# Performance work log

Hardware: AMD Instinct MI355X
Metric: run time of the kernel (lower is better)

## Reference

```python
import jax, jax.numpy as jnp
import numpy as np

N = 20000      # nodes
E = 320000     # edges (before self loops)
DIN = 64       # input feature dim
C = 256        # hidden_dim (per-head channels)
HEADS = 4
NEG_SLOPE_ATT = 0.2   # GATv2 leaky_relu slope
NEG_SLOPE = 0.01      # torch F.leaky_relu default


def setup_inputs() -> dict:
    key = jax.random.key(0)
    ks = jax.random.split(key, 32)
    def g(i, shape, fan_in):
        return jax.random.normal(ks[i], shape, jnp.float32) * (1.0 / np.sqrt(fan_in))
    inp = {}
    inp["x"] = jax.random.normal(ks[0], (N, DIN), jnp.float32)
    inp["src"] = jax.random.randint(ks[1], (E,), 0, N, jnp.int32)
    inp["dst"] = jax.random.randint(ks[2], (E,), 0, N, jnp.int32)
    # input layer
    inp["W_in"] = g(3, (DIN, C), DIN); inp["b_in"] = jnp.zeros((C,), jnp.float32)
    # conv1: in=256 -> heads=4, out=256, concat
    inp["Wl1"] = g(4, (C, HEADS * C), C); inp["bl1"] = jnp.zeros((HEADS * C,), jnp.float32)
    inp["Wr1"] = g(5, (C, HEADS * C), C); inp["br1"] = jnp.zeros((HEADS * C,), jnp.float32)
    inp["att1"] = g(6, (HEADS, C), C); inp["bias1"] = jnp.zeros((HEADS * C,), jnp.float32)
    # conv2: in=1024 -> heads=4, out=256, concat
    inp["Wl2"] = g(7, (HEADS * C, HEADS * C), HEADS * C); inp["bl2"] = jnp.zeros((HEADS * C,), jnp.float32)
    inp["Wr2"] = g(8, (HEADS * C, HEADS * C), HEADS * C); inp["br2"] = jnp.zeros((HEADS * C,), jnp.float32)
    inp["att2"] = g(9, (HEADS, C), C); inp["bias2"] = jnp.zeros((HEADS * C,), jnp.float32)
    # conv3: in=1024 -> heads=1, out=256, no concat
    inp["Wl3"] = g(10, (HEADS * C, C), HEADS * C); inp["bl3"] = jnp.zeros((C,), jnp.float32)
    inp["Wr3"] = g(11, (HEADS * C, C), HEADS * C); inp["br3"] = jnp.zeros((C,), jnp.float32)
    inp["att3"] = g(12, (1, C), C); inp["bias3"] = jnp.zeros((C,), jnp.float32)
    # output layer
    inp["W_out"] = g(13, (C, 1), C); inp["b_out"] = jnp.zeros((1,), jnp.float32)
    return inp


def _seg_softmax(scores, seg, n):
    # scores: [E, H] segment-wise softmax over dst node ids
    m = jax.ops.segment_max(scores, seg, num_segments=n)
    ex = jnp.exp(scores - m[seg])
    den = jax.ops.segment_sum(ex, seg, num_segments=n)
    return ex / den[seg]


def _gatv2(x, s, d, Wl, bl, Wr, br, att, bias, heads, concat):
    n = x.shape[0]
    c = att.shape[1]
    xl = (x @ Wl + bl).reshape(n, heads, c)  # messages (source side)
    xr = (x @ Wr + br).reshape(n, heads, c)  # target side
    e = jax.nn.leaky_relu(xl[s] + xr[d], NEG_SLOPE_ATT)          # [E, H, C]
    sc = jnp.einsum('ehc,hc->eh', e, att)                         # [E, H]
    alpha = _seg_softmax(sc, d, n)                                # [E, H]
    out = jax.ops.segment_sum(alpha[:, :, None] * xl[s], d, num_segments=n)  # [N, H, C]
    out = out.reshape(n, heads * c) if concat else out.mean(axis=1)
    return out + bias


def reference(x, src, dst, W_in, b_in, Wl1, bl1, Wr1, br1, att1, bias1,
              Wl2, bl2, Wr2, br2, att2, bias2, Wl3, bl3, Wr3, br3, att3, bias3,
              W_out, b_out):
    n = x.shape[0]
    loop = jnp.arange(n, dtype=src.dtype)
    s = jnp.concatenate([src, loop])  # add_self_loops=True (PyG default)
    d = jnp.concatenate([dst, loop])
    h = jax.nn.leaky_relu(x @ W_in + b_in, NEG_SLOPE)
    h1 = jax.nn.elu(_gatv2(h, s, d, Wl1, bl1, Wr1, br1, att1, bias1, HEADS, True))
    h2 = jax.nn.elu(_gatv2(h1, s, d, Wl2, bl2, Wr2, br2, att2, bias2, HEADS, True))
    h3 = _gatv2(h2, s, d, Wl3, bl3, Wr3, br3, att3, bias3, 1, False)
    out = jax.nn.leaky_relu(h3, NEG_SLOPE) + h
    logits = (out @ W_out + b_out).squeeze(-1)
    return logits
```

## Files before the change

kernel.cpp:

```cpp
#include <hip/hip_runtime.h>
#include <math.h>

#define NEG_ATT 0.2f
#define NEG 0.01f

typedef __attribute__((ext_vector_type(8))) short short8;
typedef __attribute__((ext_vector_type(4))) float f32x4;

static __device__ __forceinline__ float lrelu(float x, float s) { return x > 0.f ? x : s * x; }
static __device__ __forceinline__ unsigned short f2b(float f) {
  union { float f; unsigned int i; } v; v.f = f;
  unsigned int r = (v.i + 0x7fffu + ((v.i >> 16) & 1u)) >> 16;
  return (unsigned short)r;
}
static __device__ __forceinline__ void unpack8(uint4 r, float* x) {
  union { unsigned int u; float f; } t;
  t.u = r.x << 16;          x[0] = t.f;
  t.u = r.x & 0xffff0000u;  x[1] = t.f;
  t.u = r.y << 16;          x[2] = t.f;
  t.u = r.y & 0xffff0000u;  x[3] = t.f;
  t.u = r.z << 16;          x[4] = t.f;
  t.u = r.z & 0xffff0000u;  x[5] = t.f;
  t.u = r.w << 16;          x[6] = t.f;
  t.u = r.w & 0xffff0000u;  x[7] = t.f;
}
static __device__ __forceinline__ void async_copy16(const unsigned short* g, unsigned short* l) {
  __builtin_amdgcn_global_load_lds((const __attribute__((address_space(1))) unsigned int*)g,
                                   (__attribute__((address_space(3))) unsigned int*)l, 16, 0, 0);
}

__global__ void zero_int_kernel(int* __restrict__ p, int n) {
  int i = blockIdx.x * blockDim.x + threadIdx.x;
  if (i < n) p[i] = 0;
}

__global__ void hist_kernel(const int* __restrict__ dst, int* __restrict__ cnt, int E, int N) {
  int i = blockIdx.x * blockDim.x + threadIdx.x;
  int tot = E + N;
  if (i >= tot) return;
  int d = (i < E) ? dst[i] : (i - E);
  atomicAdd(&cnt[d], 1);
}

__global__ void scan_kernel(const int* __restrict__ cnt, int* __restrict__ rowptr,
                            int* __restrict__ cursor, int n) {
  __shared__ int wsum[16];
  __shared__ int carry_s;
  int t = threadIdx.x;
  int lane = t & 63, wv = t >> 6;
  if (t == 0) carry_s = 0;
  __syncthreads();
  for (int base = 0; base < n; base += 1024) {
    int i = base + t;
    int orig = (i < n) ? cnt[i] : 0;
    int v = orig;
    #pragma unroll
    for (int off = 1; off < 64; off <<= 1) {
      int u = __shfl_up(v, off);
      if (lane >= off) v += u;
    }
    if (lane == 63) wsum[wv] = v;
    __syncthreads();
    if (t < 16) {
      int s = wsum[t];
      #pragma unroll
      for (int off = 1; off < 16; off <<= 1) {
        int u = __shfl_up(s, off);
        if (t >= off) s += u;
      }
      wsum[t] = s;
    }
    __syncthreads();
    int waveoff = (wv > 0) ? wsum[wv - 1] : 0;
    int carry = carry_s;
    int excl = carry + waveoff + v - orig;
    if (i < n) { rowptr[i] = excl; cursor[i] = excl; }
    __syncthreads();
    if (t == 0) carry_s = carry + wsum[15];
    __syncthreads();
  }
  if (t == 0) rowptr[n] = carry_s;
}

__global__ void fill_kernel(const int* __restrict__ src, const int* __restrict__ dst,
                            int* __restrict__ cursor, int* __restrict__ colsrc, int E, int N) {
  int i = blockIdx.x * blockDim.x + threadIdx.x;
  int tot = E + N;
  if (i >= tot) return;
  int d, s;
  if (i < E) { d = dst[i]; s = src[i]; } else { d = i - E; s = i - E; }
  int pos = atomicAdd(&cursor[d], 1);
  colsrc[pos] = s;
}

__global__ __launch_bounds__(256) void transpose_w_bf16(
    const float* __restrict__ W, unsigned short* __restrict__ Wt, int K, int Ncol) {
  __shared__ float t[32][33];
  int n0 = blockIdx.x * 32, k0 = blockIdx.y * 32;
  int tx = threadIdx.x & 31, ty = threadIdx.x >> 5;
  #pragma unroll
  for (int i = 0; i < 4; ++i)
    t[ty + i * 8][tx] = W[(size_t)(k0 + ty + i * 8) * Ncol + n0 + tx];
  __syncthreads();
  #pragma unroll
  for (int i = 0; i < 4; ++i)
    Wt[(size_t)(n0 + ty + i * 8) * K + k0 + tx] = f2b(t[tx][ty + i * 8]);
}

__global__ void f2b_kernel(const float* __restrict__ in, unsigned short* __restrict__ out, int n) {
  int i = blockIdx.x * blockDim.x + threadIdx.x;
  if (i < n) out[i] = f2b(in[i]);
}

__global__ __launch_bounds__(256) void gemm_mfma(
    const unsigned short* __restrict__ A, const unsigned short* __restrict__ Bt,
    const float* __restrict__ bias, float* __restrict__ Cf, unsigned short* __restrict__ Cb,
    int M, int K, int ldcf, int ldcb, int act) {
  __shared__ __align__(16) unsigned short As[128][32];
  __shared__ __align__(16) unsigned short Bs[128][32];
  int tid = threadIdx.x;
  int wave = tid >> 6, lane = tid & 63;
  int wm = wave >> 1, wn = wave & 1;
  int quad = lane >> 4, l16 = lane & 15;
  int row0 = blockIdx.y * 128, col0 = blockIdx.x * 128;
  int lrow = lane >> 2, lseg = lane & 3;

  const unsigned short* gA = A + (size_t)(row0 + wave * 32 + lrow) * K + lseg * 8;
  const unsigned short* gB = Bt + (size_t)(col0 + wave * 32 + lrow) * K + lseg * 8;
  unsigned short* lA0 = &As[wave * 32][0];
  unsigned short* lA1 = &As[wave * 32 + 16][0];
  unsigned short* lB0 = &Bs[wave * 32][0];
  unsigned short* lB1 = &Bs[wave * 32 + 16][0];
  const size_t rstep = (size_t)16 * K;

  f32x4 acc[4][4];
  #pragma unroll
  for (int i = 0; i < 4; ++i)
    #pragma unroll
    for (int j = 0; j < 4; ++j)
      acc[i][j] = (f32x4){0.f, 0.f, 0.f, 0.f};

  for (int k0 = 0; k0 < K; k0 += 32) {
    async_copy16(gA + k0, lA0);
    async_copy16(gA + k0 + rstep, lA1);
    async_copy16(gB + k0, lB0);
    async_copy16(gB + k0 + rstep, lB1);
    __syncthreads();
    short8 afr[4], bfr[4];
    #pragma unroll
    for (int t = 0; t < 4; ++t) {
      afr[t] = *(const short8*)&As[wm * 64 + t * 16 + l16][quad * 8];
      bfr[t] = *(const short8*)&Bs[wn * 64 + t * 16 + l16][quad * 8];
    }
    #pragma unroll
    for (int mt = 0; mt < 4; ++mt)
      #pragma unroll
      for (int nt = 0; nt < 4; ++nt)
        acc[mt][nt] = __builtin_amdgcn_mfma_f32_16x16x32_bf16(afr[mt], bfr[nt], acc[mt][nt], 0, 0, 0);
    __syncthreads();
  }

  #pragma unroll
  for (int mt = 0; mt < 4; ++mt) {
    #pragma unroll
    for (int r = 0; r < 4; ++r) {
      int row = row0 + wm * 64 + mt * 16 + quad * 4 + r;
      if (row >= M) continue;
      #pragma unroll
      for (int nt = 0; nt < 4; ++nt) {
        int col = col0 + wn * 64 + nt * 16 + l16;
        float v = acc[mt][nt][r] + bias[col];
        if (act == 1) v = lrelu(v, NEG);
        if (Cf) Cf[(size_t)row * ldcf + col] = v;
        if (Cb) Cb[(size_t)row * ldcb + col] = f2b(v);
      }
    }
  }
}

__global__ __launch_bounds__(256) void gat_agg_h4(
    const unsigned short* __restrict__ xlr,
    const int* __restrict__ rowptr, const int* __restrict__ colsrc,
    const float* __restrict__ att, const float* __restrict__ bias,
    unsigned short* __restrict__ outb, int n) {
  const int S = 2048, XROFF = 1024;
  int d = blockIdx.x;
  if (d >= n) return;
  int hd = threadIdx.x >> 6, ln = threadIdx.x & 63;
  int half = ln >> 5, l32 = ln & 31;
  int c0 = l32 * 8;
  float a[8], a5[8], xr_[8];
  {
    float4 t0 = *(const float4*)(att + hd * 256 + c0);
    float4 t1 = *(const float4*)(att + hd * 256 + c0 + 4);
    a[0]=t0.x; a[1]=t0.y; a[2]=t0.z; a[3]=t0.w;
    a[4]=t1.x; a[5]=t1.y; a[6]=t1.z; a[7]=t1.w;
    #pragma unroll
    for (int c = 0; c < 8; ++c) a5[c] = NEG_ATT * a[c];
    uint4 r = *(const uint4*)(xlr + (size_t)d * S + XROFF + hd * 256 + c0);
    unpack8(r, xr_);
  }
  float m = -1e30f, l = 0.f, acc[8];
  #pragma unroll
  for (int c = 0; c < 8; ++c) acc[c] = 0.f;
  int beg = rowptr[d], end = rowptr[d + 1];
  for (int j = beg; j < end; j += 2) {
    int jj = j + half;
    bool valid = (jj < end);
    int s = colsrc[valid ? jj : j];
    uint4 raw = *(const uint4*)(xlr + (size_t)s * S + hd * 256 + c0);
    float x[8];
    unpack8(raw, x);
    float p = 0.f;
    #pragma unroll
    for (int c = 0; c < 8; ++c) {
      float u = x[c] + xr_[c];
      p = fmaf(u, (u > 0.f ? a[c] : a5[c]), p);
    }
    #pragma unroll
    for (int off = 16; off >= 1; off >>= 1) p += __shfl_xor(p, off);
    if (!valid) p = -1e30f;
    float nm = fmaxf(m, p);
    if (nm > m) {
      float scl = __expf(m - nm);
      l *= scl;
      #pragma unroll
      for (int c = 0; c < 8; ++c) acc[c] *= scl;
      m = nm;
    }
    float w = __expf(p - m);
    l += w;
    #pragma unroll
    for (int c = 0; c < 8; ++c) acc[c] = fmaf(w, x[c], acc[c]);
  }
  float mo = __shfl_xor(m, 32);
  float lo = __shfl_xor(l, 32);
  float M = fmaxf(m, mo);
  float sl = __expf(m - M);
  float so = __expf(mo - M);
  float L = fmaf(l, sl, lo * so);
  float inv = 1.f / L;
  float4 b0 = *(const float4*)(bias + hd * 256 + c0);
  float4 b1 = *(const float4*)(bias + hd * 256 + c0 + 4);
  float bb[8] = {b0.x, b0.y, b0.z, b0.w, b1.x, b1.y, b1.z, b1.w};
  unsigned int ou[4];
  #pragma unroll
  for (int c = 0; c < 8; ++c) {
    float po = __shfl_xor(acc[c], 32);
    float v = fmaf(acc[c], sl, po * so) * inv + bb[c];
    v = v > 0.f ? v : expm1f(v);
    unsigned int bv = (unsigned int)f2b(v);
    if (c & 1) ou[c >> 1] |= bv << 16; else ou[c >> 1] = bv;
  }
  if (half == 0) {
    uint4 o = make_uint4(ou[0], ou[1], ou[2], ou[3]);
    *(uint4*)(outb + (size_t)d * 1024 + hd * 256 + c0) = o;
  }
}

__global__ __launch_bounds__(256) void gat_agg_h1(
    const unsigned short* __restrict__ xlr,
    const int* __restrict__ rowptr, const int* __restrict__ colsrc,
    const float* __restrict__ att, const float* __restrict__ bias,
    float* __restrict__ out, int n) {
  const int S = 512, XROFF = 256;
  int wv = threadIdx.x >> 6, ln = threadIdx.x & 63;
  int d = blockIdx.x * 4 + wv;
  if (d >= n) return;
  int half = ln >> 5, l32 = ln & 31;
  int c0 = l32 * 8;
  float a[8], a5[8], xr_[8];
  {
    float4 t0 = *(const float4*)(att + c0);
    float4 t1 = *(const float4*)(att + c0 + 4);
    a[0]=t0.x; a[1]=t0.y; a[2]=t0.z; a[3]=t0.w;
    a[4]=t1.x; a[5]=t1.y; a[6]=t1.z; a[7]=t1.w;
    #pragma unroll
    for (int c = 0; c < 8; ++c) a5[c] = NEG_ATT * a[c];
    uint4 r = *(const uint4*)(xlr + (size_t)d * S + XROFF + c0);
    unpack8(r, xr_);
  }
  float m = -1e30f, l = 0.f, acc[8];
  #pragma unroll
  for (int c = 0; c < 8; ++c) acc[c] = 0.f;
  int beg = rowptr[d], end = rowptr[d + 1];
  for (int j = beg; j < end; j += 2) {
    int jj = j + half;
    bool valid = (jj < end);
    int s = colsrc[valid ? jj : j];
    uint4 raw = *(const uint4*)(xlr + (size_t)s * S + c0);
    float x[8];
    unpack8(raw, x);
    float p = 0.f;
    #pragma unroll
    for (int c = 0; c < 8; ++c) {
      float u = x[c] + xr_[c];
      p = fmaf(u, (u > 0.f ? a[c] : a5[c]), p);
    }
    #pragma unroll
    for (int off = 16; off >= 1; off >>= 1) p += __shfl_xor(p, off);
    if (!valid) p = -1e30f;
    float nm = fmaxf(m, p);
    if (nm > m) {
      float scl = __expf(m - nm);
      l *= scl;
      #pragma unroll
      for (int c = 0; c < 8; ++c) acc[c] *= scl;
      m = nm;
    }
    float w = __expf(p - m);
    l += w;
    #pragma unroll
    for (int c = 0; c < 8; ++c) acc[c] = fmaf(w, x[c], acc[c]);
  }
  float mo = __shfl_xor(m, 32);
  float lo = __shfl_xor(l, 32);
  float M = fmaxf(m, mo);
  float sl = __expf(m - M);
  float so = __expf(mo - M);
  float L = fmaf(l, sl, lo * so);
  float inv = 1.f / L;
  float4 b0 = *(const float4*)(bias + c0);
  float4 b1 = *(const float4*)(bias + c0 + 4);
  float bb[8] = {b0.x, b0.y, b0.z, b0.w, b1.x, b1.y, b1.z, b1.w};
  float ov[8];
  #pragma unroll
  for (int c = 0; c < 8; ++c) {
    float po = __shfl_xor(acc[c], 32);
    ov[c] = fmaf(acc[c], sl, po * so) * inv + bb[c];
  }
  if (half == 0) {
    float4 o0 = {ov[0], ov[1], ov[2], ov[3]};
    float4 o1 = {ov[4], ov[5], ov[6], ov[7]};
    *(float4*)(out + (size_t)d * 256 + c0) = o0;
    *(float4*)(out + (size_t)d * 256 + c0 + 4) = o1;
  }
}

__global__ __launch_bounds__(256) void final_logits(
    const float* __restrict__ h3, const float* __restrict__ h,
    const float* __restrict__ Wout, const float* __restrict__ bout,
    float* __restrict__ out, int n) {
  int wv = threadIdx.x >> 6, ln = threadIdx.x & 63;
  int node = blockIdx.x * 4 + wv;
  if (node >= n) return;
  int c0 = ln * 4;
  float4 a = *(const float4*)(h3 + (size_t)node * 256 + c0);
  float4 b = *(const float4*)(h + (size_t)node * 256 + c0);
  float4 w = *(const float4*)(Wout + c0);
  float vx = lrelu(a.x, NEG) + b.x;
  float vy = lrelu(a.y, NEG) + b.y;
  float vz = lrelu(a.z, NEG) + b.z;
  float vw = lrelu(a.w, NEG) + b.w;
  float v = vx * w.x + vy * w.y + vz * w.z + vw * w.w;
  #pragma unroll
  for (int off = 32; off >= 1; off >>= 1) v += __shfl_xor(v, off);
  if (ln == 0) out[node] = v + bout[0];
}

extern "C" void kernel_launch(void* const* d_in, const int* in_sizes, int n_in,
                              void* d_out, int out_size, void* d_ws, size_t ws_size,
                              hipStream_t stream) {
  const float* x    = (const float*)d_in[0];
  const int*   src  = (const int*)d_in[1];
  const int*   dst  = (const int*)d_in[2];
  const float* W_in = (const float*)d_in[3];
  const float* b_in = (const float*)d_in[4];
  const float* Wl1 = (const float*)d_in[5];  const float* bl1 = (const float*)d_in[6];
  const float* Wr1 = (const float*)d_in[7];  const float* br1 = (const float*)d_in[8];
  const float* att1 = (const float*)d_in[9]; const float* bias1 = (const float*)d_in[10];
  const float* Wl2 = (const float*)d_in[11]; const float* bl2 = (const float*)d_in[12];
  const float* Wr2 = (const float*)d_in[13]; const float* br2 = (const float*)d_in[14];
  const float* att2 = (const float*)d_in[15]; const float* bias2 = (const float*)d_in[16];
  const float* Wl3 = (const float*)d_in[17]; const float* bl3 = (const float*)d_in[18];
  const float* Wr3 = (const float*)d_in[19]; const float* br3 = (const float*)d_in[20];
  const float* att3 = (const float*)d_in[21]; const float* bias3 = (const float*)d_in[22];
  const float* W_out = (const float*)d_in[23]; const float* b_out = (const float*)d_in[24];

  const int N = in_sizes[0] / 64;
  const int E = in_sizes[1];
  const int NP = ((N + 127) / 128) * 128;
  float* out = (float*)d_out;

  char* p = (char*)d_ws;
  float* h   = (float*)p;            p += (size_t)N * 256 * 4;
  float* h3  = (float*)p;            p += (size_t)N * 256 * 4;
  unsigned short* xbf  = (unsigned short*)p; p += (size_t)NP * 64 * 2;
  unsigned short* hbf  = (unsigned short*)p; p += (size_t)NP * 256 * 2;
  unsigned short* h1bf = (unsigned short*)p; p += (size_t)NP * 1024 * 2;
  unsigned short* h2bf = (unsigned short*)p; p += (size_t)NP * 1024 * 2;
  unsigned short* xlr  = (unsigned short*)p; p += (size_t)N * 2048 * 2;
  unsigned short* WtIn  = (unsigned short*)p; p += (size_t)256 * 64 * 2;
  unsigned short* WtLR1 = (unsigned short*)p; p += (size_t)2048 * 256 * 2;
  unsigned short* WtLR2 = (unsigned short*)p; p += (size_t)2048 * 1024 * 2;
  unsigned short* WtLR3 = (unsigned short*)p; p += (size_t)512 * 1024 * 2;
  float* bLR1 = (float*)p;           p += (size_t)2048 * 4;
  float* bLR2 = (float*)p;           p += (size_t)2048 * 4;
  float* bLR3 = (float*)p;           p += (size_t)512 * 4;
  int* cnt    = (int*)p;             p += (size_t)N * 4;
  int* cursor = (int*)p;             p += (size_t)N * 4;
  int* rowptr = (int*)p;             p += (size_t)(N + 1) * 4;
  int* colsrc = (int*)p;

  const int tot = E + N;
  dim3 blk(256);

  zero_int_kernel<<<(N + 255) / 256, blk, 0, stream>>>(cnt, N);
  hist_kernel<<<(tot + 255) / 256, blk, 0, stream>>>(dst, cnt, E, N);
  scan_kernel<<<1, 1024, 0, stream>>>(cnt, rowptr, cursor, N);
  fill_kernel<<<(tot + 255) / 256, blk, 0, stream>>>(src, dst, cursor, colsrc, E, N);

  transpose_w_bf16<<<dim3(8, 2), blk, 0, stream>>>(W_in, WtIn, 64, 256);
  transpose_w_bf16<<<dim3(32, 8), blk, 0, stream>>>(Wl1, WtLR1, 256, 1024);
  transpose_w_bf16<<<dim3(32, 8), blk, 0, stream>>>(Wr1, WtLR1 + (size_t)1024 * 256, 256, 1024);
  transpose_w_bf16<<<dim3(32, 32), blk, 0, stream>>>(Wl2, WtLR2, 1024, 1024);
  transpose_w_bf16<<<dim3(32, 32), blk, 0, stream>>>(Wr2, WtLR2 + (size_t)1024 * 1024, 1024, 1024);
  transpose_w_bf16<<<dim3(8, 32), blk, 0, stream>>>(Wl3, WtLR3, 1024, 256);
  transpose_w_bf16<<<dim3(8, 32), blk, 0, stream>>>(Wr3, WtLR3 + (size_t)256 * 1024, 1024, 256);
  f2b_kernel<<<(N * 64 + 255) / 256, blk, 0, stream>>>(x, xbf, N * 64);

  hipMemcpyAsync(bLR1, bl1, 1024 * 4, hipMemcpyDeviceToDevice, stream);
  hipMemcpyAsync(bLR1 + 1024, br1, 1024 * 4, hipMemcpyDeviceToDevice, stream);
  hipMemcpyAsync(bLR2, bl2, 1024 * 4, hipMemcpyDeviceToDevice, stream);
  hipMemcpyAsync(bLR2 + 1024, br2, 1024 * 4, hipMemcpyDeviceToDevice, stream);
  hipMemcpyAsync(bLR3, bl3, 256 * 4, hipMemcpyDeviceToDevice, stream);
  hipMemcpyAsync(bLR3 + 256, br3, 256 * 4, hipMemcpyDeviceToDevice, stream);

  int gy = NP / 128;
  int gagg4 = N;
  int gagg1 = (N + 3) / 4;

  gemm_mfma<<<dim3(2, gy), blk, 0, stream>>>(xbf, WtIn, b_in, h, hbf, N, 64, 256, 256, 1);

  gemm_mfma<<<dim3(16, gy), blk, 0, stream>>>(hbf, WtLR1, bLR1, nullptr, xlr, N, 256, 0, 2048, 0);
  gat_agg_h4<<<gagg4, blk, 0, stream>>>(xlr, rowptr, colsrc, att1, bias1, h1bf, N);

  gemm_mfma<<<dim3(16, gy), blk, 0, stream>>>(h1bf, WtLR2, bLR2, nullptr, xlr, N, 1024, 0, 2048, 0);
  gat_agg_h4<<<gagg4, blk, 0, stream>>>(xlr, rowptr, colsrc, att2, bias2, h2bf, N);

  gemm_mfma<<<dim3(4, gy), blk, 0, stream>>>(h2bf, WtLR3, bLR3, nullptr, xlr, N, 1024, 0, 512, 0);
  gat_agg_h1<<<gagg1, blk, 0, stream>>>(xlr, rowptr, colsrc, att3, bias3, h3, N);

  final_logits<<<gagg1, blk, 0, stream>>>(h3, h, W_out, b_out, out, N);
}
```

Measured before the change: 803.5 us.

## Register-prefetch GEMM tiles with XOR-swizzled LDS layout instead of direct-to-LDS loads

```diff
diff --git a/kernel.cpp b/kernel.cpp
--- a/kernel.cpp
+++ b/kernel.cpp
@@ -23,10 +23,6 @@
   t.u = r.z & 0xffff0000u;  x[5] = t.f;
   t.u = r.w << 16;          x[6] = t.f;
   t.u = r.w & 0xffff0000u;  x[7] = t.f;
-}
-static __device__ __forceinline__ void async_copy16(const unsigned short* g, unsigned short* l) {
-  __builtin_amdgcn_global_load_lds((const __attribute__((address_space(1))) unsigned int*)g,
-                                   (__attribute__((address_space(3))) unsigned int*)l, 16, 0, 0);
 }
 
 __global__ void zero_int_kernel(int* __restrict__ p, int n) {
@@ -116,22 +112,21 @@
     const unsigned short* __restrict__ A, const unsigned short* __restrict__ Bt,
     const float* __restrict__ bias, float* __restrict__ Cf, unsigned short* __restrict__ Cb,
     int M, int K, int ldcf, int ldcb, int act) {
-  __shared__ __align__(16) unsigned short As[128][32];
-  __shared__ __align__(16) unsigned short Bs[128][32];
+  __shared__ __align__(16) unsigned short As[128 * 32];
+  __shared__ __align__(16) unsigned short Bs[128 * 32];
   int tid = threadIdx.x;
   int wave = tid >> 6, lane = tid & 63;
   int wm = wave >> 1, wn = wave & 1;
   int quad = lane >> 4, l16 = lane & 15;
   int row0 = blockIdx.y * 128, col0 = blockIdx.x * 128;
-  int lrow = lane >> 2, lseg = lane & 3;
-
-  const unsigned short* gA = A + (size_t)(row0 + wave * 32 + lrow) * K + lseg * 8;
-  const unsigned short* gB = Bt + (size_t)(col0 + wave * 32 + lrow) * K + lseg * 8;
-  unsigned short* lA0 = &As[wave * 32][0];
-  unsigned short* lA1 = &As[wave * 32 + 16][0];
-  unsigned short* lB0 = &Bs[wave * 32][0];
-  unsigned short* lB1 = &Bs[wave * 32 + 16][0];
-  const size_t rstep = (size_t)16 * K;
+  int r0 = tid >> 2, seg0 = tid & 3;
+  int swz0 = r0 * 32 + ((seg0 ^ ((r0 >> 1) & 3)) * 8);
+  int swz1 = swz0 + 64 * 32;
+  int chunk = (quad ^ ((l16 >> 1) & 3)) * 8;
+
+  const unsigned short* gA = A + (size_t)(row0 + r0) * K + seg0 * 8;
+  const unsigned short* gB = Bt + (size_t)(col0 + r0) * K + seg0 * 8;
+  const size_t rstep = (size_t)64 * K;
 
   f32x4 acc[4][4];
   #pragma unroll
@@ -140,17 +135,29 @@
     for (int j = 0; j < 4; ++j)
       acc[i][j] = (f32x4){0.f, 0.f, 0.f, 0.f};
 
+  uint4 sa0 = *(const uint4*)(gA);
+  uint4 sa1 = *(const uint4*)(gA + rstep);
+  uint4 sb0 = *(const uint4*)(gB);
+  uint4 sb1 = *(const uint4*)(gB + rstep);
+
   for (int k0 = 0; k0 < K; k0 += 32) {
-    async_copy16(gA + k0, lA0);
-    async_copy16(gA + k0 + rstep, lA1);
-    async_copy16(gB + k0, lB0);
-    async_copy16(gB + k0 + rstep, lB1);
-    __syncthreads();
+    *(uint4*)&As[swz0] = sa0;
+    *(uint4*)&As[swz1] = sa1;
+    *(uint4*)&Bs[swz0] = sb0;
+    *(uint4*)&Bs[swz1] = sb1;
+    __syncthreads();
+    int kn = k0 + 32;
+    if (kn < K) {
+      sa0 = *(const uint4*)(gA + kn);
+      sa1 = *(const uint4*)(gA + kn + rstep);
+      sb0 = *(const uint4*)(gB + kn);
+      sb1 = *(const uint4*)(gB + kn + rstep);
+    }
     short8 afr[4], bfr[4];
     #pragma unroll
     for (int t = 0; t < 4; ++t) {
-      afr[t] = *(const short8*)&As[wm * 64 + t * 16 + l16][quad * 8];
-      bfr[t] = *(const short8*)&Bs[wn * 64 + t * 16 + l16][quad * 8];
+      afr[t] = *(const short8*)&As[(wm * 64 + t * 16 + l16) * 32 + chunk];
+      bfr[t] = *(const short8*)&Bs[(wn * 64 + t * 16 + l16) * 32 + chunk];
     }
     #pragma unroll
     for (int mt = 0; mt < 4; ++mt)
```

Result: faster. 784.2 us (-2.4%).
